# Kernel optimization log

Hardware: AMD Instinct MI355X
Metric: run time of the kernel (lower is better)

## Reference

```python
import jax, jax.numpy as jnp
import numpy as np

NUM_WIRES = 12
NUM_LAYERS = 3
BATCH = 8192
DIM = 2 ** NUM_WIRES


def _rx(theta):
    # RX(t) = [[cos(t/2), -i sin(t/2)], [-i sin(t/2), cos(t/2)]]; theta scalar or (B,)
    h = theta * 0.5
    c = jnp.cos(h).astype(jnp.complex64)
    s = (-1j) * jnp.sin(h).astype(jnp.complex64)
    return jnp.stack([jnp.stack([c, s], -1), jnp.stack([s, c], -1)], -2)


def _ry(theta):
    # RY(t) = [[cos(t/2), -sin(t/2)], [sin(t/2), cos(t/2)]]
    h = theta * 0.5
    c = jnp.cos(h)
    s = jnp.sin(h)
    m = jnp.stack([jnp.stack([c, -s], -1), jnp.stack([s, c], -1)], -2)
    return m.astype(jnp.complex64)


def _apply_1q(psi, mat, wire):
    # psi: (B, 2**n); pennylane wire 0 is most significant bit
    B = psi.shape[0]
    s = psi.reshape(B, 2 ** wire, 2, -1)
    if mat.ndim == 2:
        out = jnp.einsum('ij,bajc->baic', mat, s)
    else:  # per-sample gate, mat: (B, 2, 2)
        out = jnp.einsum('bij,bajc->baic', mat, s)
    return out.reshape(B, -1)


def _cnot(psi, control, target):
    B = psi.shape[0]
    a, b = (control, target) if control < target else (target, control)
    s = psi.reshape(B, 2 ** a, 2, 2 ** (b - a - 1), 2, -1)
    if control == a:
        # control on axis 2, flip target (axis 4) where control bit == 1
        s = s.at[:, :, 1].set(s[:, :, 1, :, ::-1])
    else:
        # control on axis 4, flip target (axis 2) where control bit == 1
        s = s.at[:, :, :, :, 1].set(s[:, :, ::-1, :, 1])
    return s.reshape(B, -1)


def _circuit(angles, weights):
    # angles: (B, n) per-sample input rotations; weights: (L, n, 2)
    B = angles.shape[0]
    n = NUM_WIRES
    psi = jnp.zeros((B, DIM), jnp.complex64).at[:, 0].set(1.0)
    for i in range(n):
        psi = _apply_1q(psi, _rx(angles[:, i]), i)
        psi = _apply_1q(psi, _ry(angles[:, i]), i)
    for l in range(NUM_LAYERS):
        for i in range(n):
            psi = _apply_1q(psi, _rx(weights[l, i, 0]), i)
            psi = _apply_1q(psi, _ry(weights[l, i, 1]), i)
        for i in range(n - 1):
            psi = _cnot(psi, i, i + 1)
        psi = _cnot(psi, n - 1, 0)
    probs = (psi.real ** 2 + psi.imag ** 2).reshape((B,) + (2,) * n)
    zs = []
    for i in range(n):
        other = tuple(j + 1 for j in range(n) if j != i)
        p = probs.sum(other)  # (B, 2)
        zs.append(p[:, 0] - p[:, 1])  # <Z_i> = P(0) - P(1)
    return jnp.stack(zs, -1)  # (B, n)


def setup_inputs() -> dict:
    key = jax.random.key(0)
    ks = jax.random.split(key, 5)
    return {
        'state_real': jax.random.normal(ks[0], (BATCH, DIM), jnp.float32),
        'state_imag': jax.random.normal(ks[1], (BATCH, DIM), jnp.float32),
        'weights': jax.random.normal(ks[2], (NUM_LAYERS, NUM_WIRES, 2), jnp.float32),
        'head_w': jax.random.normal(ks[3], (1, NUM_WIRES), jnp.float32) / np.sqrt(NUM_WIRES).astype(np.float32),
        'head_b': jax.random.normal(ks[4], (1,), jnp.float32),
    }


def reference(state_real, state_imag, weights, head_w, head_b):
    angles = jnp.arctan2(state_imag[:, :NUM_WIRES], state_real[:, :NUM_WIRES])  # (B, n)
    q = _circuit(angles, weights)  # (B, n)
    return (q @ head_w.T + head_b).squeeze(-1)  # (B,)
```

## Files before the change

### kernel.cpp

```cpp
#include <hip/hip_runtime.h>

typedef __fp16 h2v __attribute__((ext_vector_type(2)));
typedef _Float16 f16x8 __attribute__((ext_vector_type(8)));
typedef float f32x4 __attribute__((ext_vector_type(4)));

#define BLK 256
#define BATCH 8192

struct M12 { unsigned r[12]; };

constexpr M12 mp_matrix() {
  M12 m{};
  for (int p = 0; p <= 10; ++p) m.r[p] = (0xFFFu >> p) << p;
  m.r[11] = 0x7FFu;
  return m;
}
constexpr M12 MP = mp_matrix();

constexpr unsigned mv(const M12 m, unsigned v) {
  unsigned y = 0;
  for (int p = 0; p < 12; ++p)
    y |= (unsigned)(__builtin_popcount(m.r[p] & v) & 1) << p;
  return y;
}
constexpr M12 mmul(const M12 a, const M12 b) {
  M12 c{};
  for (int p = 0; p < 12; ++p) {
    unsigned acc = 0;
    for (int q = 0; q < 12; ++q)
      if ((a.r[p] >> q) & 1u) acc ^= b.r[q];
    c.r[p] = acc;
  }
  return c;
}
constexpr M12 minv(const M12 a0) {
  unsigned a[12] = {}, v[12] = {};
  for (int i = 0; i < 12; ++i) { a[i] = a0.r[i]; v[i] = 1u << i; }
  for (int c = 0; c < 12; ++c) {
    int piv = c;
    while (!((a[piv] >> c) & 1u)) ++piv;
    unsigned ta = a[piv], tv = v[piv];
    a[piv] = a[c]; v[piv] = v[c]; a[c] = ta; v[c] = tv;
    for (int r2 = 0; r2 < 12; ++r2)
      if (r2 != c && ((a[r2] >> c) & 1u)) { a[r2] ^= a[c]; v[r2] ^= v[c]; }
  }
  M12 out{};
  for (int i = 0; i < 12; ++i) out.r[i] = v[i];
  return out;
}
constexpr unsigned colq(const M12 m, int q) {
  unsigned c = 0;
  for (int p = 0; p < 12; ++p) c |= ((m.r[p] >> q) & 1u) << p;
  return c;
}
constexpr M12 from_cols(const unsigned (&c)[12]) {
  M12 m{};
  for (int p = 0; p < 12; ++p) {
    unsigned row = 0;
    for (int j = 0; j < 12; ++j) row |= ((c[j] >> p) & 1u) << j;
    m.r[p] = row;
  }
  return m;
}
constexpr M12 mk_id() { M12 m{}; for (int p = 0; p < 12; ++p) m.r[p] = 1u << p; return m; }
constexpr M12 MID = mk_id();
constexpr M12 MPI = minv(MP);

constexpr bool meq(const M12 a, const M12 b) {
  for (int p = 0; p < 12; ++p) if (a.r[p] != b.r[p]) return false;
  return true;
}
static_assert(meq(mmul(MP, MPI), MID), "P inverse");

struct Frame { M12 A, Ai; };
constexpr Frame FID{MID, MID};
constexpr Frame absorb(const Frame f) { return Frame{ mmul(MP, f.A), mmul(f.Ai, MPI) }; }
constexpr Frame apply_tau(const Frame f, const M12 t) {
  return Frame{ mmul(f.A, minv(t)), mmul(t, f.Ai) };
}

constexpr M12 make_tau_W(const Frame f, const int* qs, const unsigned* tg) {
  unsigned S[12] = {}, D[12] = {}, rows[4] = {};
  for (int i = 0; i < 4; ++i) {
    S[i] = colq(f.Ai, qs[i]);
    D[i] = tg[i];
    rows[i] = f.A.r[qs[i]];
  }
  unsigned R[4] = {rows[0], rows[1], rows[2], rows[3]};
  int pivcol[4] = {-1, -1, -1, -1};
  int nr = 0;
  for (int c = 0; c < 12 && nr < 4; ++c) {
    int pr = -1;
    for (int r2 = nr; r2 < 4; ++r2) if ((R[r2] >> c) & 1u) { pr = r2; break; }
    if (pr < 0) continue;
    unsigned tmp = R[nr]; R[nr] = R[pr]; R[pr] = tmp;
    for (int r2 = 0; r2 < 4; ++r2)
      if (r2 != nr && ((R[r2] >> c) & 1u)) R[r2] ^= R[nr];
    pivcol[nr] = c; ++nr;
  }
  int cnt = 4;
  for (int j = 0; j < 12; ++j) {
    bool isp = false;
    for (int k = 0; k < nr; ++k) if (pivcol[k] == j) isp = true;
    if (isp) continue;
    unsigned v = 1u << j;
    for (int k = 0; k < nr; ++k) if ((R[k] >> j) & 1u) v |= 1u << pivcol[k];
    S[cnt] = v;
    ++cnt;
  }
  for (int i = 4; i < 12; ++i) D[i] = 1u << i;
  return mmul(from_cols(D), minv(from_cols(S)));
}
constexpr bool chk_group(const Frame f, const int* qs, const unsigned* tg) {
  for (int i = 0; i < 4; ++i) if (colq(f.Ai, qs[i]) != tg[i]) return false;
  return true;
}

constexpr int QA[4] = {11, 10, 9, 8};
constexpr int QB[4] = {7, 6, 5, 4};
constexpr int QC[4] = {3, 2, 1, 0};
constexpr unsigned T4[4] = {8u, 4u, 2u, 1u};

constexpr Frame F1  = absorb(FID);
constexpr M12  S2a = make_tau_W(F1,  QA, T4);
constexpr Frame F2a = apply_tau(F1, S2a);
constexpr M12  S2b = make_tau_W(F2a, QB, T4);
constexpr Frame F2b = apply_tau(F2a, S2b);
constexpr M12  S2c = make_tau_W(F2b, QC, T4);
constexpr Frame F2c = apply_tau(F2b, S2c);
constexpr Frame F3  = absorb(F2c);
constexpr M12  S3a = make_tau_W(F3,  QA, T4);
constexpr Frame F3a = apply_tau(F3, S3a);
constexpr M12  S3b = make_tau_W(F3a, QB, T4);
constexpr Frame F3b = apply_tau(F3a, S3b);
constexpr M12  S3c = make_tau_W(F3b, QC, T4);
constexpr Frame F3c = apply_tau(F3b, S3c);
constexpr Frame F4  = absorb(F3c);

static_assert(chk_group(F2a, QA, T4), "G2a");
static_assert(chk_group(F2b, QB, T4), "G2b");
static_assert(chk_group(F2c, QC, T4), "G2c");
static_assert(chk_group(F3a, QA, T4), "G3a");
static_assert(chk_group(F3b, QB, T4), "G3b");
static_assert(chk_group(F3c, QC, T4), "G3c");
static_assert(F2a.A.r[11] == 8u && F2a.A.r[10] == 4u && F2a.A.r[9] == 2u && F2a.A.r[8] == 1u, "rows2a");
static_assert(F2b.A.r[7]  == 8u && F2b.A.r[6]  == 4u && F2b.A.r[5] == 2u && F2b.A.r[4] == 1u, "rows2b");
static_assert(F2c.A.r[3]  == 8u && F2c.A.r[2]  == 4u && F2c.A.r[1] == 2u && F2c.A.r[0] == 1u, "rows2c");
static_assert(F3a.A.r[11] == 8u && F3a.A.r[10] == 4u && F3a.A.r[9] == 2u && F3a.A.r[8] == 1u, "rows3a");
static_assert(F3b.A.r[7]  == 8u && F3b.A.r[6]  == 4u && F3b.A.r[5] == 2u && F3b.A.r[4] == 1u, "rows3b");
static_assert(F3c.A.r[3]  == 8u && F3c.A.r[2]  == 4u && F3c.A.r[1] == 2u && F3c.A.r[0] == 1u, "rows3c");

struct BSw { unsigned mk[7]; };
constexpr unsigned bswap(const BSw& b, unsigned v) {
  unsigned o = v;
  for (int k = 0; k < 7; ++k)
    if ((v >> (5 + k)) & 1u) o ^= b.mk[k];
  return o;
}
constexpr int rank5(const unsigned* v, int n) {
  unsigned basis[5] = {};
  int r = 0;
  for (int i = 0; i < n; ++i) {
    unsigned x = v[i];
    for (int b = 4; b >= 0; --b) {
      if (!((x >> b) & 1u)) continue;
      if (basis[b]) x ^= basis[b];
      else { basis[b] = x; ++r; break; }
    }
  }
  return r;
}
constexpr int readrank(const BSw& b) {
  unsigned v[5] = { bswap(b, 16u) & 0x1Cu, bswap(b, 32u) & 0x1Cu,
                    bswap(b, 64u) & 0x1Cu, bswap(b, 128u) & 0x1Cu,
                    bswap(b, 8u) & 0x1Cu };
  return rank5(v, 5);
}
constexpr int wrankf(const BSw& b, const unsigned* tv) {
  unsigned v[6] = {};
  for (int k = 0; k < 6; ++k) v[k] = bswap(b, tv[k]) & 0x1Fu;
  return rank5(v, 6);
}
constexpr BSw find_bsw(const M12 T, bool dpass) {
  unsigned src[6] = {16u, 32u, 64u, 128u, dpass ? 4u : 256u, dpass ? 8u : 512u};
  unsigned tv[6] = {};
  for (int k = 0; k < 6; ++k) tv[k] = mv(T, src[k]);
  BSw b{};
  b.mk[0] = 4u;
  int bw = wrankf(b, tv);
  for (int s = 0; s < 2; ++s)
    for (int k = 0; k < 7; ++k) {
      unsigned bestv = b.mk[k];
      for (unsigned v = 0; v < 8; ++v) {
        b.mk[k] = v << 2;
        if (readrank(b) < 3) continue;
        const int wr = wrankf(b, tv);
        if (wr > bw) { bw = wr; bestv = v << 2; }
      }
      b.mk[k] = bestv;
    }
  return b;
}
constexpr BSw B0 = find_bsw(S2a, false);
constexpr BSw B1 = find_bsw(S2b, true);
constexpr BSw B2 = find_bsw(S2c, true);
constexpr BSw B3 = find_bsw(S3a, true);
constexpr BSw B4 = find_bsw(S3b, true);
constexpr BSw B5 = find_bsw(S3c, true);
static_assert(readrank(B0) == 3 && readrank(B1) == 3 && readrank(B2) == 3 &&
              readrank(B3) == 3 && readrank(B4) == 3 && readrank(B5) == 3, "rr");

struct PT {
  unsigned wc[16];
  unsigned wlb[6], wwb[2];
  unsigned rlb[5], rwb[2];
  unsigned rm[2];
};
constexpr PT mk_pt(const M12 T, const BSw b, bool dpass) {
  PT t{};
  for (int v = 0; v < 16; ++v) {
    const unsigned p = dpass ? ((((unsigned)v >> 2) << 8) | ((unsigned)v & 3u))
                             : (unsigned)v;
    t.wc[v] = bswap(b, mv(T, p));
  }
  unsigned src[6] = {16u, 32u, 64u, 128u, dpass ? 4u : 256u, dpass ? 8u : 512u};
  for (int k = 0; k < 6; ++k) t.wlb[k] = bswap(b, mv(T, src[k]));
  t.wwb[0] = bswap(b, mv(T, 1024u));
  t.wwb[1] = bswap(b, mv(T, 2048u));
  t.rlb[0] = bswap(b, 16u);  t.rlb[1] = bswap(b, 32u);
  t.rlb[2] = bswap(b, 64u);  t.rlb[3] = bswap(b, 128u);
  t.rlb[4] = bswap(b, 8u);
  t.rwb[0] = bswap(b, 1024u); t.rwb[1] = bswap(b, 2048u);
  t.rm[0] = bswap(b, 256u);   t.rm[1] = bswap(b, 512u);
  return t;
}
constexpr PT RT[6] = { mk_pt(S2a, B0, false), mk_pt(S2b, B1, true),
                       mk_pt(S2c, B2, true),  mk_pt(S3a, B3, true),
                       mk_pt(S3b, B4, true),  mk_pt(S3c, B5, true) };

template<int PI>
__device__ __forceinline__ unsigned wbase_of(const int lane, const int w) {
  unsigned wb = 0u;
  #pragma unroll
  for (int k = 0; k < 6; ++k) wb ^= ((lane >> k) & 1) ? RT[PI].wlb[k] : 0u;
  wb ^= (w & 1) ? RT[PI].wwb[0] : 0u;
  wb ^= (w & 2) ? RT[PI].wwb[1] : 0u;
  return wb;
}
template<int PI>
__device__ __forceinline__ unsigned rbase_of(const int lane, const int w) {
  unsigned rb = 0u;
  #pragma unroll
  for (int k = 0; k < 4; ++k) rb ^= ((lane >> k) & 1) ? RT[PI].rlb[k] : 0u;
  rb ^= ((lane >> 4) & 1) ? RT[PI].rlb[4] : 0u;
  rb ^= (w & 1) ? RT[PI].rwb[0] : 0u;
  rb ^= (w & 2) ? RT[PI].rwb[1] : 0u;
  return rb;
}

template<int PI>
__device__ __forceinline__ void do_pass(f32x4 (&D1)[4], f32x4 (&D2)[4],
                                        const unsigned* sb, const uint4* Am4,
                                        const int lane, const int w,
                                        const unsigned sel) {
  const uint4 a1u = Am4[(PI * 2 + 0) * 64 + lane];
  const uint4 a2u = Am4[(PI * 2 + 1) * 64 + lane];
  const f16x8 A1f = __builtin_bit_cast(f16x8, a1u);
  const f16x8 A2f = __builtin_bit_cast(f16x8, a2u);
  const unsigned rb = rbase_of<PI>(lane, w);
  const f32x4 z4 = {0.f, 0.f, 0.f, 0.f};
  #pragma unroll
  for (int m = 0; m < 4; ++m) {
    const unsigned mo = rb ^ ((m & 1) ? RT[PI].rm[0] : 0u)
                           ^ ((m & 2) ? RT[PI].rm[1] : 0u);
    const uint4 lo = *(const uint4*)(sb + mo);
    const uint4 hi = *(const uint4*)(sb + (mo ^ 4u));
    uint4 bw;
    bw.x = __builtin_amdgcn_perm(lo.y, lo.x, sel);
    bw.y = __builtin_amdgcn_perm(lo.w, lo.z, sel);
    bw.z = __builtin_amdgcn_perm(hi.y, hi.x, sel);
    bw.w = __builtin_amdgcn_perm(hi.w, hi.z, sel);
    const f16x8 Bf = __builtin_bit_cast(f16x8, bw);
    D1[m] = __builtin_amdgcn_mfma_f32_16x16x32_f16(A1f, Bf, z4, 0, 0, 0);
    D2[m] = __builtin_amdgcn_mfma_f32_16x16x32_f16(A2f, Bf, z4, 0, 0, 0);
  }
}

template<int PI>
__device__ __forceinline__ void write_pass(const f32x4 (&D1)[4],
                                           const f32x4 (&D2)[4],
                                           unsigned* sb, const int lane,
                                           const int w) {
  const unsigned wb = wbase_of<PI>(lane, w);
  h2v* sh = (h2v*)sb;
  #pragma unroll
  for (int m = 0; m < 4; ++m)
    #pragma unroll
    for (int r = 0; r < 4; ++r)
      sh[wb ^ RT[PI].wc[(m << 2) | r]] =
          __builtin_amdgcn_cvt_pkrtz(D1[m][r], D2[m][r]);
}

__device__ __forceinline__ void gentry(const float4 g, const int rb,
                                       const int kb, float& re, float& im) {
  re = rb ? (kb ? g.x : g.z) : (kb ? -g.z : g.x);
  im = rb ? (kb ? -g.y : g.w) : (kb ? g.w : g.y);
}

__global__ __launch_bounds__(BLK, 4) void qsim_kernel(
    const float* __restrict__ sr, const float* __restrict__ si,
    const float* __restrict__ wts, const float* __restrict__ hw,
    const float* __restrict__ hb, float* __restrict__ out) {
  __shared__ __align__(16) unsigned sbuf[4096];
  __shared__ __align__(16) unsigned Amat[3072];
  __shared__ float4 gt4[24];
  __shared__ float4 qv[12];
  __shared__ float xacc[4];

  const int t = threadIdx.x;
  const int lane = t & 63;
  const int w = t >> 6;
  const int s = blockIdx.x;

  if (t < 24) {
    const int l = 1 + t / 12, i = t % 12;
    const float a  = wts[(l * 12 + i) * 2 + 0] * 0.5f;
    const float bb = wts[(l * 12 + i) * 2 + 1] * 0.5f;
    float sa, ca, sb2, cb;
    sincosf(a, &sa, &ca);
    sincosf(bb, &sb2, &cb);
    gt4[t] = make_float4(cb * ca, sb2 * sa, sb2 * ca, -cb * sa);
  }
  if (t >= 64 && t < 76) {
    const int i = t - 64;
    const float ang = atan2f(si[(size_t)s * 4096 + i],
                             sr[(size_t)s * 4096 + i]) * 0.5f;
    float sn, cs;
    sincosf(ang, &sn, &cs);
    const float e0r = cs * cs, e0i = sn * sn, e1r = sn * cs, e1i = -sn * cs;
    const float a  = wts[i * 2 + 0] * 0.5f;
    const float bb = wts[i * 2 + 1] * 0.5f;
    float sa, ca, sb2, cb;
    sincosf(a, &sa, &ca);
    sincosf(bb, &sb2, &cb);
    const float g00r = cb * ca,  g00i = sb2 * sa, g01r = -sb2 * ca, g01i = -cb * sa;
    const float g10r = sb2 * ca, g10i = -cb * sa, g11r = cb * ca,   g11i = -sb2 * sa;
    const float q0r = g00r * e0r - g00i * e0i + g01r * e1r - g01i * e1i;
    const float q0i = g00r * e0i + g00i * e0r + g01r * e1i + g01i * e1r;
    const float q1r = g10r * e0r - g10i * e0i + g11r * e1r - g11i * e1i;
    const float q1i = g10r * e0i + g10i * e0r + g11r * e1i + g11i * e1r;
    qv[i] = make_float4(q0r, q0i, q1r, q1i);
  }
  __syncthreads();

  #pragma unroll
  for (int rep = 0; rep < 3; ++rep) {
    const int idx = t + rep * BLK;
    const int pass = idx >> 7;
    const int mat  = (idx >> 6) & 1;
    const int lw   = idx & 63;
    const int r    = lw & 15;
    const int ks   = lw >> 4;
    const int imf  = ks >> 1;
    const float4 g0 = gt4[pass * 4 + 0];
    const float4 g1 = gt4[pass * 4 + 1];
    const float4 g2 = gt4[pass * 4 + 2];
    const float4 g3 = gt4[pass * 4 + 3];
    float b3r, b3i;
    gentry(g0, (r >> 3) & 1, ks & 1, b3r, b3i);
    float t2r[2], t2i[2];
    #pragma unroll
    for (int k2 = 0; k2 < 2; ++k2) {
      float cr, ci;
      gentry(g1, (r >> 2) & 1, k2, cr, ci);
      t2r[k2] = b3r * cr - b3i * ci;
      t2i[k2] = b3r * ci + b3i * cr;
    }
    float t1r[4], t1i[4];
    #pragma unroll
    for (int k2 = 0; k2 < 2; ++k2)
      #pragma unroll
      for (int k1 = 0; k1 < 2; ++k1) {
        float cr, ci;
        gentry(g2, (r >> 1) & 1, k1, cr, ci);
        t1r[k2 * 2 + k1] = t2r[k2] * cr - t2i[k2] * ci;
        t1i[k2 * 2 + k1] = t2r[k2] * ci + t2i[k2] * cr;
      }
    float ev[8];
    #pragma unroll
    for (int j = 0; j < 8; ++j) {
      float cr, ci;
      gentry(g3, r & 1, j & 1, cr, ci);
      const int h2 = j >> 1;
      const float er = t1r[h2] * cr - t1i[h2] * ci;
      const float ei = t1r[h2] * ci + t1i[h2] * cr;
      ev[j] = (mat == 0) ? (imf ? -ei : er) : (imf ? er : ei);
    }
    const int base = ((pass * 2 + mat) * 64 + lw) * 4;
    #pragma unroll
    for (int q = 0; q < 4; ++q) {
      const h2v pk = __builtin_amdgcn_cvt_pkrtz(ev[2 * q], ev[2 * q + 1]);
      Amat[base + q] = __builtin_bit_cast(unsigned, pk);
    }
  }

  float ar[16], ai[16];
  {
    const float4* q = qv;
    float Lr, Li;
    { const float4 q0 = q[0]; const int b0 = (w >> 1) & 1;
      Lr = b0 ? q0.z : q0.x; Li = b0 ? q0.w : q0.y; }
    { const float4 q1 = q[1]; const int b1 = w & 1;
      const float fr = b1 ? q1.z : q1.x, fi = b1 ? q1.w : q1.y;
      const float nr = Lr * fr - Li * fi, ni = Lr * fi + Li * fr;
      Lr = nr; Li = ni; }
    #pragma unroll
    for (int i = 2; i <= 7; ++i) {
      const float4 qq = q[i];
      const int bit = (lane >> (7 - i)) & 1;
      const float fr = bit ? qq.z : qq.x, fi = bit ? qq.w : qq.y;
      const float nr = Lr * fr - Li * fi, ni = Lr * fi + Li * fr;
      Lr = nr; Li = ni;
    }
    float LTr[4], LTi[4];
    { const float4 q8 = q[8], q9 = q[9];
      #pragma unroll
      for (int m = 0; m < 4; ++m) {
        const float xr2 = (m & 2) ? q8.z : q8.x, xi2 = (m & 2) ? q8.w : q8.y;
        const float yr = (m & 1) ? q9.z : q9.x, yi = (m & 1) ? q9.w : q9.y;
        const float tr = xr2 * yr - xi2 * yi, ti = xr2 * yi + xi2 * yr;
        LTr[m] = Lr * tr - Li * ti;
        LTi[m] = Lr * ti + Li * tr;
      } }
    float tbr[4], tbi[4];
    { const float4 qA = q[10], qB2 = q[11];
      #pragma unroll
      for (int m = 0; m < 4; ++m) {
        const float xr2 = (m & 2) ? qA.z : qA.x, xi2 = (m & 2) ? qA.w : qA.y;
        const float yr = (m & 1) ? qB2.z : qB2.x, yi = (m & 1) ? qB2.w : qB2.y;
        tbr[m] = xr2 * yr - xi2 * yi;
        tbi[m] = xr2 * yi + xi2 * yr;
      } }
    #pragma unroll
    for (int l = 0; l < 16; ++l) {
      ar[l] = LTr[l >> 2] * tbr[l & 3] - LTi[l >> 2] * tbi[l & 3];
      ai[l] = LTr[l >> 2] * tbi[l & 3] + LTi[l >> 2] * tbr[l & 3];
    }
  }

  {
    const unsigned wb = wbase_of<0>(lane, w);
    h2v* sh = (h2v*)sbuf;
    #pragma unroll
    for (int l = 0; l < 16; ++l)
      sh[wb ^ RT[0].wc[l]] = __builtin_amdgcn_cvt_pkrtz(ar[l], ai[l]);
  }
  __syncthreads();

  const unsigned sel = (lane & 32) ? 0x07060302u : 0x05040100u;
  const uint4* Am4 = (const uint4*)Amat;
  f32x4 D1[4], D2[4];

  do_pass<0>(D1, D2, sbuf, Am4, lane, w, sel);
  __syncthreads();
  write_pass<1>(D1, D2, sbuf, lane, w);
  __syncthreads();
  do_pass<1>(D1, D2, sbuf, Am4, lane, w, sel);
  __syncthreads();
  write_pass<2>(D1, D2, sbuf, lane, w);
  __syncthreads();
  do_pass<2>(D1, D2, sbuf, Am4, lane, w, sel);
  __syncthreads();
  write_pass<3>(D1, D2, sbuf, lane, w);
  __syncthreads();
  do_pass<3>(D1, D2, sbuf, Am4, lane, w, sel);
  __syncthreads();
  write_pass<4>(D1, D2, sbuf, lane, w);
  __syncthreads();
  do_pass<4>(D1, D2, sbuf, Am4, lane, w, sel);
  __syncthreads();
  write_pass<5>(D1, D2, sbuf, lane, w);
  __syncthreads();
  do_pass<5>(D1, D2, sbuf, Am4, lane, w, sel);

  const unsigned pbase = ((unsigned)w << 10) | ((unsigned)(lane & 15) << 4) |
                         ((unsigned)((lane >> 4) & 3) << 2);
  float hp[12];
  #pragma unroll
  for (int i = 0; i < 12; ++i) {
    const unsigned R = F4.A.r[11 - i];
    const float h = hw[i];
    hp[i] = (__popc(pbase & R & 0xCFCu) & 1) ? -h : h;
  }
  float c[16];
  #pragma unroll
  for (int v = 0; v < 16; ++v) c[v] = 0.f;
  #pragma unroll
  for (int i = 0; i < 12; ++i) {
    const unsigned R = F4.A.r[11 - i];
    const int mu = (int)((((R >> 8) & 3u) << 2) | (R & 3u));
    c[mu] += hp[i];
  }
  #pragma unroll
  for (int bb = 1; bb < 16; bb <<= 1)
    #pragma unroll
    for (int v = 0; v < 16; ++v)
      if (!(v & bb)) {
        const float x = c[v], y = c[v | bb];
        c[v] = x + y;
        c[v | bb] = x - y;
      }
  float acc = 0.f;
  #pragma unroll
  for (int m = 0; m < 4; ++m)
    #pragma unroll
    for (int r = 0; r < 4; ++r)
      acc += (D1[m][r] * D1[m][r] + D2[m][r] * D2[m][r]) * c[(m << 2) | r];
  #pragma unroll
  for (int off = 1; off < 64; off <<= 1) acc += __shfl_xor(acc, off, 64);

  if (lane == 0) xacc[w] = acc;
  __syncthreads();
  if (t == 0) out[s] = xacc[0] + xacc[1] + xacc[2] + xacc[3] + hb[0];
}

extern "C" void kernel_launch(void* const* d_in, const int* in_sizes, int n_in,
                              void* d_out, int out_size, void* d_ws, size_t ws_size,
                              hipStream_t stream) {
  const float* sr  = (const float*)d_in[0];
  const float* si  = (const float*)d_in[1];
  const float* wts = (const float*)d_in[2];
  const float* hw  = (const float*)d_in[3];
  const float* hb  = (const float*)d_in[4];
  float* out = (float*)d_out;
  qsim_kernel<<<BATCH, BLK, 0, stream>>>(sr, si, wts, hw, hb, out);
}
```

Before: 101.7 us.

## Double-buffer LDS state, keep gate matrices in registers, search better tau frames

Each pass now alternates between two LDS state buffers, which drops one block barrier per pass. Every lane builds its six passes' packed fp16 gate fragments directly in registers, so the shared Amat table and its per-pass loads are gone. The compile-time frame transforms now try eight rotations of the null-space basis and keep the one whose bank-swizzle score is highest, aiming for fewer LDS bank conflicts. The cost is 48 extra VGPRs for the A fragments plus a second 16 KB LDS buffer, which may lower occupancy, and more redundant per-lane matrix setup work.

```diff
diff --git a/kernel.cpp b/kernel.cpp
--- a/kernel.cpp
+++ b/kernel.cpp
@@ -78,77 +78,6 @@
 constexpr Frame apply_tau(const Frame f, const M12 t) {
   return Frame{ mmul(f.A, minv(t)), mmul(t, f.Ai) };
 }
-
-constexpr M12 make_tau_W(const Frame f, const int* qs, const unsigned* tg) {
-  unsigned S[12] = {}, D[12] = {}, rows[4] = {};
-  for (int i = 0; i < 4; ++i) {
-    S[i] = colq(f.Ai, qs[i]);
-    D[i] = tg[i];
-    rows[i] = f.A.r[qs[i]];
-  }
-  unsigned R[4] = {rows[0], rows[1], rows[2], rows[3]};
-  int pivcol[4] = {-1, -1, -1, -1};
-  int nr = 0;
-  for (int c = 0; c < 12 && nr < 4; ++c) {
-    int pr = -1;
-    for (int r2 = nr; r2 < 4; ++r2) if ((R[r2] >> c) & 1u) { pr = r2; break; }
-    if (pr < 0) continue;
-    unsigned tmp = R[nr]; R[nr] = R[pr]; R[pr] = tmp;
-    for (int r2 = 0; r2 < 4; ++r2)
-      if (r2 != nr && ((R[r2] >> c) & 1u)) R[r2] ^= R[nr];
-    pivcol[nr] = c; ++nr;
-  }
-  int cnt = 4;
-  for (int j = 0; j < 12; ++j) {
-    bool isp = false;
-    for (int k = 0; k < nr; ++k) if (pivcol[k] == j) isp = true;
-    if (isp) continue;
-    unsigned v = 1u << j;
-    for (int k = 0; k < nr; ++k) if ((R[k] >> j) & 1u) v |= 1u << pivcol[k];
-    S[cnt] = v;
-    ++cnt;
-  }
-  for (int i = 4; i < 12; ++i) D[i] = 1u << i;
-  return mmul(from_cols(D), minv(from_cols(S)));
-}
-constexpr bool chk_group(const Frame f, const int* qs, const unsigned* tg) {
-  for (int i = 0; i < 4; ++i) if (colq(f.Ai, qs[i]) != tg[i]) return false;
-  return true;
-}
-
-constexpr int QA[4] = {11, 10, 9, 8};
-constexpr int QB[4] = {7, 6, 5, 4};
-constexpr int QC[4] = {3, 2, 1, 0};
-constexpr unsigned T4[4] = {8u, 4u, 2u, 1u};
-
-constexpr Frame F1  = absorb(FID);
-constexpr M12  S2a = make_tau_W(F1,  QA, T4);
-constexpr Frame F2a = apply_tau(F1, S2a);
-constexpr M12  S2b = make_tau_W(F2a, QB, T4);
-constexpr Frame F2b = apply_tau(F2a, S2b);
-constexpr M12  S2c = make_tau_W(F2b, QC, T4);
-constexpr Frame F2c = apply_tau(F2b, S2c);
-constexpr Frame F3  = absorb(F2c);
-constexpr M12  S3a = make_tau_W(F3,  QA, T4);
-constexpr Frame F3a = apply_tau(F3, S3a);
-constexpr M12  S3b = make_tau_W(F3a, QB, T4);
-constexpr Frame F3b = apply_tau(F3a, S3b);
-constexpr M12  S3c = make_tau_W(F3b, QC, T4);
-constexpr Frame F3c = apply_tau(F3b, S3c);
-constexpr Frame F4  = absorb(F3c);
-
-static_assert(chk_group(F2a, QA, T4), "G2a");
-static_assert(chk_group(F2b, QB, T4), "G2b");
-static_assert(chk_group(F2c, QC, T4), "G2c");
-static_assert(chk_group(F3a, QA, T4), "G3a");
-static_assert(chk_group(F3b, QB, T4), "G3b");
-static_assert(chk_group(F3c, QC, T4), "G3c");
-static_assert(F2a.A.r[11] == 8u && F2a.A.r[10] == 4u && F2a.A.r[9] == 2u && F2a.A.r[8] == 1u, "rows2a");
-static_assert(F2b.A.r[7]  == 8u && F2b.A.r[6]  == 4u && F2b.A.r[5] == 2u && F2b.A.r[4] == 1u, "rows2b");
-static_assert(F2c.A.r[3]  == 8u && F2c.A.r[2]  == 4u && F2c.A.r[1] == 2u && F2c.A.r[0] == 1u, "rows2c");
-static_assert(F3a.A.r[11] == 8u && F3a.A.r[10] == 4u && F3a.A.r[9] == 2u && F3a.A.r[8] == 1u, "rows3a");
-static_assert(F3b.A.r[7]  == 8u && F3b.A.r[6]  == 4u && F3b.A.r[5] == 2u && F3b.A.r[4] == 1u, "rows3b");
-static_assert(F3c.A.r[3]  == 8u && F3c.A.r[2]  == 4u && F3c.A.r[1] == 2u && F3c.A.r[0] == 1u, "rows3c");
 
 struct BSw { unsigned mk[7]; };
 constexpr unsigned bswap(const BSw& b, unsigned v) {
@@ -201,6 +130,99 @@
     }
   return b;
 }
+
+constexpr M12 mtw_c(const Frame f, const int* qs, const unsigned* tg, int c) {
+  unsigned S[12] = {}, D[12] = {}, rows[4] = {};
+  for (int i = 0; i < 4; ++i) {
+    S[i] = colq(f.Ai, qs[i]);
+    D[i] = tg[i];
+    rows[i] = f.A.r[qs[i]];
+  }
+  unsigned R[4] = {rows[0], rows[1], rows[2], rows[3]};
+  int pivcol[4] = {-1, -1, -1, -1};
+  int nr = 0;
+  for (int cc = 0; cc < 12 && nr < 4; ++cc) {
+    int pr = -1;
+    for (int r2 = nr; r2 < 4; ++r2) if ((R[r2] >> cc) & 1u) { pr = r2; break; }
+    if (pr < 0) continue;
+    unsigned tmp = R[nr]; R[nr] = R[pr]; R[pr] = tmp;
+    for (int r2 = 0; r2 < 4; ++r2)
+      if (r2 != nr && ((R[r2] >> cc) & 1u)) R[r2] ^= R[nr];
+    pivcol[nr] = cc; ++nr;
+  }
+  unsigned nb[8] = {};
+  int nc = 0;
+  for (int j = 0; j < 12; ++j) {
+    bool isp = false;
+    for (int k = 0; k < nr; ++k) if (pivcol[k] == j) isp = true;
+    if (isp) continue;
+    unsigned v = 1u << j;
+    for (int k = 0; k < nr; ++k) if ((R[k] >> j) & 1u) v |= 1u << pivcol[k];
+    nb[nc] = v;
+    ++nc;
+  }
+  for (int j = 0; j < 8; ++j) {
+    S[4 + j] = nb[(j + c) & 7];
+    D[4 + j] = 1u << (4 + j);
+  }
+  return mmul(from_cols(D), minv(from_cols(S)));
+}
+constexpr int tau_score(const M12 T, bool dpass) {
+  const BSw b = find_bsw(T, dpass);
+  unsigned src[6] = {16u, 32u, 64u, 128u, dpass ? 4u : 256u, dpass ? 8u : 512u};
+  unsigned tv[6] = {};
+  for (int k = 0; k < 6; ++k) tv[k] = mv(T, src[k]);
+  return wrankf(b, tv);
+}
+constexpr M12 pick_tau(const Frame f, const int* qs, const unsigned* tg,
+                       bool dpass) {
+  int bc = 0, bs = -1;
+  for (int c = 0; c < 8; ++c) {
+    const M12 T = mtw_c(f, qs, tg, c);
+    const int sc2 = tau_score(T, dpass);
+    if (sc2 > bs) { bs = sc2; bc = c; }
+  }
+  return mtw_c(f, qs, tg, bc);
+}
+constexpr bool chk_group(const Frame f, const int* qs, const unsigned* tg) {
+  for (int i = 0; i < 4; ++i) if (colq(f.Ai, qs[i]) != tg[i]) return false;
+  return true;
+}
+
+constexpr int QA[4] = {11, 10, 9, 8};
+constexpr int QB[4] = {7, 6, 5, 4};
+constexpr int QC[4] = {3, 2, 1, 0};
+constexpr unsigned T4[4] = {8u, 4u, 2u, 1u};
+
+constexpr Frame F1  = absorb(FID);
+constexpr M12  S2a = pick_tau(F1,  QA, T4, false);
+constexpr Frame F2a = apply_tau(F1, S2a);
+constexpr M12  S2b = pick_tau(F2a, QB, T4, true);
+constexpr Frame F2b = apply_tau(F2a, S2b);
+constexpr M12  S2c = pick_tau(F2b, QC, T4, true);
+constexpr Frame F2c = apply_tau(F2b, S2c);
+constexpr Frame F3  = absorb(F2c);
+constexpr M12  S3a = pick_tau(F3,  QA, T4, true);
+constexpr Frame F3a = apply_tau(F3, S3a);
+constexpr M12  S3b = pick_tau(F3a, QB, T4, true);
+constexpr Frame F3b = apply_tau(F3a, S3b);
+constexpr M12  S3c = pick_tau(F3b, QC, T4, true);
+constexpr Frame F3c = apply_tau(F3b, S3c);
+constexpr Frame F4  = absorb(F3c);
+
+static_assert(chk_group(F2a, QA, T4), "G2a");
+static_assert(chk_group(F2b, QB, T4), "G2b");
+static_assert(chk_group(F2c, QC, T4), "G2c");
+static_assert(chk_group(F3a, QA, T4), "G3a");
+static_assert(chk_group(F3b, QB, T4), "G3b");
+static_assert(chk_group(F3c, QC, T4), "G3c");
+static_assert(F2a.A.r[11] == 8u && F2a.A.r[10] == 4u && F2a.A.r[9] == 2u && F2a.A.r[8] == 1u, "rows2a");
+static_assert(F2b.A.r[7]  == 8u && F2b.A.r[6]  == 4u && F2b.A.r[5] == 2u && F2b.A.r[4] == 1u, "rows2b");
+static_assert(F2c.A.r[3]  == 8u && F2c.A.r[2]  == 4u && F2c.A.r[1] == 2u && F2c.A.r[0] == 1u, "rows2c");
+static_assert(F3a.A.r[11] == 8u && F3a.A.r[10] == 4u && F3a.A.r[9] == 2u && F3a.A.r[8] == 1u, "rows3a");
+static_assert(F3b.A.r[7]  == 8u && F3b.A.r[6]  == 4u && F3b.A.r[5] == 2u && F3b.A.r[4] == 1u, "rows3b");
+static_assert(F3c.A.r[3]  == 8u && F3c.A.r[2]  == 4u && F3c.A.r[1] == 2u && F3c.A.r[0] == 1u, "rows3c");
+
 constexpr BSw B0 = find_bsw(S2a, false);
 constexpr BSw B1 = find_bsw(S2b, true);
 constexpr BSw B2 = find_bsw(S2c, true);
@@ -260,11 +282,10 @@
 
 template<int PI>
 __device__ __forceinline__ void do_pass(f32x4 (&D1)[4], f32x4 (&D2)[4],
-                                        const unsigned* sb, const uint4* Am4,
+                                        const unsigned* sb,
+                                        const uint4 a1u, const uint4 a2u,
                                         const int lane, const int w,
                                         const unsigned sel) {
-  const uint4 a1u = Am4[(PI * 2 + 0) * 64 + lane];
-  const uint4 a2u = Am4[(PI * 2 + 1) * 64 + lane];
   const f16x8 A1f = __builtin_bit_cast(f16x8, a1u);
   const f16x8 A2f = __builtin_bit_cast(f16x8, a2u);
   const unsigned rb = rbase_of<PI>(lane, w);
@@ -311,8 +332,7 @@
     const float* __restrict__ sr, const float* __restrict__ si,
     const float* __restrict__ wts, const float* __restrict__ hw,
     const float* __restrict__ hb, float* __restrict__ out) {
-  __shared__ __align__(16) unsigned sbuf[4096];
-  __shared__ __align__(16) unsigned Amat[3072];
+  __shared__ __align__(16) unsigned sbuf[2][4096];
   __shared__ float4 gt4[24];
   __shared__ float4 qv[12];
   __shared__ float xacc[4];
@@ -353,59 +373,64 @@
   }
   __syncthreads();
 
-  #pragma unroll
-  for (int rep = 0; rep < 3; ++rep) {
-    const int idx = t + rep * BLK;
-    const int pass = idx >> 7;
-    const int mat  = (idx >> 6) & 1;
-    const int lw   = idx & 63;
-    const int r    = lw & 15;
-    const int ks   = lw >> 4;
-    const int imf  = ks >> 1;
-    const float4 g0 = gt4[pass * 4 + 0];
-    const float4 g1 = gt4[pass * 4 + 1];
-    const float4 g2 = gt4[pass * 4 + 2];
-    const float4 g3 = gt4[pass * 4 + 3];
-    float b3r, b3i;
-    gentry(g0, (r >> 3) & 1, ks & 1, b3r, b3i);
-    float t2r[2], t2i[2];
+  uint4 A1u[6], A2u[6];
+  {
+    const int row = lane & 15;
+    const int ks  = lane >> 4;
+    const int imf = ks >> 1;
+    const int kb3 = ks & 1;
     #pragma unroll
-    for (int k2 = 0; k2 < 2; ++k2) {
-      float cr, ci;
-      gentry(g1, (r >> 2) & 1, k2, cr, ci);
-      t2r[k2] = b3r * cr - b3i * ci;
-      t2i[k2] = b3r * ci + b3i * cr;
+    for (int pass = 0; pass < 6; ++pass) {
+      const float4 g0 = gt4[pass * 4 + 0];
+      const float4 g1 = gt4[pass * 4 + 1];
+      const float4 g2 = gt4[pass * 4 + 2];
+      const float4 g3 = gt4[pass * 4 + 3];
+      float b3r, b3i;
+      gentry(g0, (row >> 3) & 1, kb3, b3r, b3i);
+      float t2r[2], t2i[2];
+      #pragma unroll
+      for (int k2 = 0; k2 < 2; ++k2) {
+        float cr, ci;
+        gentry(g1, (row >> 2) & 1, k2, cr, ci);
+        t2r[k2] = b3r * cr - b3i * ci;
+        t2i[k2] = b3r * ci + b3i * cr;
+      }
+      float t1r[4], t1i[4];
+      #pragma unroll
+      for (int k2 = 0; k2 < 2; ++k2)
+        #pragma unroll
+        for (int k1 = 0; k1 < 2; ++k1) {
+          float cr, ci;
+          gentry(g2, (row >> 1) & 1, k1, cr, ci);
+          t1r[k2 * 2 + k1] = t2r[k2] * cr - t2i[k2] * ci;
+          t1i[k2 * 2 + k1] = t2r[k2] * ci + t2i[k2] * cr;
+        }
+      float evr[8], evi[8];
+      #pragma unroll
+      for (int j = 0; j < 8; ++j) {
+        float cr, ci;
+        gentry(g3, row & 1, j & 1, cr, ci);
+        const int h2 = j >> 1;
+        evr[j] = t1r[h2] * cr - t1i[h2] * ci;
+        evi[j] = t1r[h2] * ci + t1i[h2] * cr;
+      }
+      unsigned u1[4], u2[4];
+      #pragma unroll
+      for (int q = 0; q < 4; ++q) {
+        const h2v p1 = imf ? __builtin_amdgcn_cvt_pkrtz(-evi[2 * q], -evi[2 * q + 1])
+                           : __builtin_amdgcn_cvt_pkrtz(evr[2 * q], evr[2 * q + 1]);
+        const h2v p2 = imf ? __builtin_amdgcn_cvt_pkrtz(evr[2 * q], evr[2 * q + 1])
+                           : __builtin_amdgcn_cvt_pkrtz(evi[2 * q], evi[2 * q + 1]);
+        u1[q] = __builtin_bit_cast(unsigned, p1);
+        u2[q] = __builtin_bit_cast(unsigned, p2);
+      }
+      A1u[pass] = make_uint4(u1[0], u1[1], u1[2], u1[3]);
+      A2u[pass] = make_uint4(u2[0], u2[1], u2[2], u2[3]);
     }
-    float t1r[4], t1i[4];
-    #pragma unroll
-    for (int k2 = 0; k2 < 2; ++k2)
-      #pragma unroll
-      for (int k1 = 0; k1 < 2; ++k1) {
-        float cr, ci;
-        gentry(g2, (r >> 1) & 1, k1, cr, ci);
-        t1r[k2 * 2 + k1] = t2r[k2] * cr - t2i[k2] * ci;
-        t1i[k2 * 2 + k1] = t2r[k2] * ci + t2i[k2] * cr;
-      }
-    float ev[8];
-    #pragma unroll
-    for (int j = 0; j < 8; ++j) {
-      float cr, ci;
-      gentry(g3, r & 1, j & 1, cr, ci);
-      const int h2 = j >> 1;
-      const float er = t1r[h2] * cr - t1i[h2] * ci;
-      const float ei = t1r[h2] * ci + t1i[h2] * cr;
-      ev[j] = (mat == 0) ? (imf ? -ei : er) : (imf ? er : ei);
-    }
-    const int base = ((pass * 2 + mat) * 64 + lw) * 4;
-    #pragma unroll
-    for (int q = 0; q < 4; ++q) {
-      const h2v pk = __builtin_amdgcn_cvt_pkrtz(ev[2 * q], ev[2 * q + 1]);
-      Amat[base + q] = __builtin_bit_cast(unsigned, pk);
-    }
-  }
-
-  float ar[16], ai[16];
+  }
+
   {
+    float ar[16], ai[16];
     const float4* q = qv;
     float Lr, Li;
     { const float4 q0 = q[0]; const int b0 = (w >> 1) & 1;
@@ -441,47 +466,36 @@
         tbr[m] = xr2 * yr - xi2 * yi;
         tbi[m] = xr2 * yi + xi2 * yr;
       } }
+    const unsigned wb = wbase_of<0>(lane, w);
+    h2v* sh = (h2v*)sbuf[0];
     #pragma unroll
     for (int l = 0; l < 16; ++l) {
-      ar[l] = LTr[l >> 2] * tbr[l & 3] - LTi[l >> 2] * tbi[l & 3];
-      ai[l] = LTr[l >> 2] * tbi[l & 3] + LTi[l >> 2] * tbr[l & 3];
+      const float arl = LTr[l >> 2] * tbr[l & 3] - LTi[l >> 2] * tbi[l & 3];
+      const float ail = LTr[l >> 2] * tbi[l & 3] + LTi[l >> 2] * tbr[l & 3];
+      sh[wb ^ RT[0].wc[l]] = __builtin_amdgcn_cvt_pkrtz(arl, ail);
     }
   }
-
-  {
-    const unsigned wb = wbase_of<0>(lane, w);
-    h2v* sh = (h2v*)sbuf;
-    #pragma unroll
-    for (int l = 0; l < 16; ++l)
-      sh[wb ^ RT[0].wc[l]] = __builtin_amdgcn_cvt_pkrtz(ar[l], ai[l]);
-  }
   __syncthreads();
 
   const unsigned sel = (lane & 32) ? 0x07060302u : 0x05040100u;
-  const uint4* Am4 = (const uint4*)Amat;
   f32x4 D1[4], D2[4];
 
-  do_pass<0>(D1, D2, sbuf, Am4, lane, w, sel);
-  __syncthreads();
-  write_pass<1>(D1, D2, sbuf, lane, w);
-  __syncthreads();
-  do_pass<1>(D1, D2, sbuf, Am4, lane, w, sel);
-  __syncthreads();
-  write_pass<2>(D1, D2, sbuf, lane, w);
-  __syncthreads();
-  do_pass<2>(D1, D2, sbuf, Am4, lane, w, sel);
-  __syncthreads();
-  write_pass<3>(D1, D2, sbuf, lane, w);
-  __syncthreads();
-  do_pass<3>(D1, D2, sbuf, Am4, lane, w, sel);
-  __syncthreads();
-  write_pass<4>(D1, D2, sbuf, lane, w);
-  __syncthreads();
-  do_pass<4>(D1, D2, sbuf, Am4, lane, w, sel);
-  __syncthreads();
-  write_pass<5>(D1, D2, sbuf, lane, w);
-  __syncthreads();
-  do_pass<5>(D1, D2, sbuf, Am4, lane, w, sel);
+  do_pass<0>(D1, D2, sbuf[0], A1u[0], A2u[0], lane, w, sel);
+  write_pass<1>(D1, D2, sbuf[1], lane, w);
+  __syncthreads();
+  do_pass<1>(D1, D2, sbuf[1], A1u[1], A2u[1], lane, w, sel);
+  write_pass<2>(D1, D2, sbuf[0], lane, w);
+  __syncthreads();
+  do_pass<2>(D1, D2, sbuf[0], A1u[2], A2u[2], lane, w, sel);
+  write_pass<3>(D1, D2, sbuf[1], lane, w);
+  __syncthreads();
+  do_pass<3>(D1, D2, sbuf[1], A1u[3], A2u[3], lane, w, sel);
+  write_pass<4>(D1, D2, sbuf[0], lane, w);
+  __syncthreads();
+  do_pass<4>(D1, D2, sbuf[0], A1u[4], A2u[4], lane, w, sel);
+  write_pass<5>(D1, D2, sbuf[1], lane, w);
+  __syncthreads();
+  do_pass<5>(D1, D2, sbuf[1], A1u[5], A2u[5], lane, w, sel);
 
   const unsigned pbase = ((unsigned)w << 10) | ((unsigned)(lane & 15) << 4) |
                          ((unsigned)((lane >> 4) & 3) << 2);
```

After: 102.4 us. Within noise of the previous version (+0.7%).
